# Kernel optimization log

Measured on AMD Instinct MI355X. Metric: run time of the kernel, lower is better.

Reference implementation:

```python
import jax, jax.numpy as jnp
import numpy as np

H = 32          # num_attention_heads
KVH = 8         # num_key_value_heads
D = 2048        # hidden_size
HD = D // H     # attention_head_size = 64
REP = H // KVH  # queries per kv head = 4


def setup_inputs() -> dict:
    key = jax.random.key(0)
    ks = jax.random.split(key, 7)
    s = 0.02
    return {
        "hidden_states": jax.random.normal(ks[0], (2, 2048, D), dtype=jnp.float32),
        "Wq": jax.random.normal(ks[1], (D, D), dtype=jnp.float32) * s,
        "bq": jax.random.normal(ks[2], (D,), dtype=jnp.float32) * s,
        "Wk": jax.random.normal(ks[3], (D, KVH * HD), dtype=jnp.float32) * s,
        "bk": jax.random.normal(ks[4], (KVH * HD,), dtype=jnp.float32) * s,
        "Wv": jax.random.normal(ks[5], (D, KVH * HD), dtype=jnp.float32) * s,
        "bv": jax.random.normal(ks[6], (KVH * HD,), dtype=jnp.float32) * s,
    }


def _split_heads(x, n_heads):
    # [B, S, n_heads*HD] -> [B, n_heads, S, HD]
    b, s, _ = x.shape
    return x.reshape(b, s, n_heads, HD).transpose(0, 2, 1, 3)


def reference(hidden_states, Wq, bq, Wk, bk, Wv, bv):
    b, s, _ = hidden_states.shape
    q = _split_heads(hidden_states @ Wq + bq, H)          # [B,H,S,HD]
    k = _split_heads(hidden_states @ Wk + bk, KVH)        # [B,KVH,S,HD]
    v = _split_heads(hidden_states @ Wv + bv, KVH)
    # repeat KV heads to match query heads (q_idx // REP -> kv_idx)
    k = jnp.repeat(k, REP, axis=1)                         # [B,H,S,HD]
    v = jnp.repeat(v, REP, axis=1)
    scores = jnp.einsum("bhqd,bhkd->bhqk", q, k) / jnp.sqrt(jnp.float32(HD))
    probs = jax.nn.softmax(scores, axis=-1)
    ctx = jnp.einsum("bhqk,bhkd->bhqd", probs, v)          # [B,H,S,HD]
    ctx = ctx.transpose(0, 2, 1, 3).reshape(b, s, H * HD)
    return ctx
```

## Files before the change

### kernel.cpp

```cpp
#include <hip/hip_runtime.h>
#include <hip/hip_bf16.h>

#define NH 32
#define NKVH 8
#define DMODEL 2048
#define HDIM 64
#define NB 2
#define SEQ 2048
#define MROWS (NB*SEQ)
#define NQ 2048
#define NKV 512
#define NTOT 3072
#define NT (SEQ/64)

typedef __bf16 bf16x4 __attribute__((ext_vector_type(4)));
typedef __bf16 bf16x8 __attribute__((ext_vector_type(8)));
typedef float  f32x2  __attribute__((ext_vector_type(2)));
typedef float  f32x4  __attribute__((ext_vector_type(4)));
typedef float  f32x16 __attribute__((ext_vector_type(16)));
typedef unsigned u32x2 __attribute__((ext_vector_type(2)));
typedef unsigned u32x4 __attribute__((ext_vector_type(4)));

__device__ inline __bf16 f2bf(float f) {
    unsigned u = __builtin_bit_cast(unsigned, f);
    u += 0x7fff + ((u >> 16) & 1);
    unsigned short s = (unsigned short)(u >> 16);
    return __builtin_bit_cast(__bf16, s);
}

__device__ inline unsigned pack2bf(float a, float b) {
    unsigned ua = __builtin_bit_cast(unsigned, a);
    ua += 0x7fff + ((ua >> 16) & 1);
    unsigned ub = __builtin_bit_cast(unsigned, b);
    ub += 0x7fff + ((ub >> 16) & 1);
    return (ua >> 16) | (ub & 0xffff0000u);
}

__device__ inline void gload_lds16(const void* g, void* l) {
    __builtin_amdgcn_global_load_lds(
        (const __attribute__((address_space(1))) void*)g,
        (__attribute__((address_space(3))) void*)l, 16, 0, 0);
}

__device__ inline float max3f(float a, float b, float c) {
    float r;
    asm("v_max3_f32 %0, %1, %2, %3" : "=v"(r) : "v"(a), "v"(b), "v"(c));
    return r;
}

__device__ inline float cross_max32(float x) {
#if __has_builtin(__builtin_amdgcn_permlane32_swap)
    unsigned xu = __builtin_bit_cast(unsigned, x);
    u32x2 r = __builtin_amdgcn_permlane32_swap(xu, xu, false, false);
    return fmaxf(__builtin_bit_cast(float, r[0]), __builtin_bit_cast(float, r[1]));
#else
    return fmaxf(x, __shfl_xor(x, 32));
#endif
}

__global__ __launch_bounds__(256)
void cvt_hs(const float* __restrict__ Hs, __bf16* __restrict__ Ab)
{
    size_t idx = ((size_t)blockIdx.x * 256 + threadIdx.x) * 8;
    f32x4 a = *reinterpret_cast<const f32x4*>(Hs + idx);
    f32x4 b = *reinterpret_cast<const f32x4*>(Hs + idx + 4);
    u32x4 w;
    w[0] = pack2bf(a[0], a[1]); w[1] = pack2bf(a[2], a[3]);
    w[2] = pack2bf(b[0], b[1]); w[3] = pack2bf(b[2], b[3]);
    *reinterpret_cast<u32x4*>((char*)Ab + idx * 2) = w;
}

__global__ __launch_bounds__(256)
void transpose_w(const float* __restrict__ Wq,
                 const float* __restrict__ Wk,
                 const float* __restrict__ Wv,
                 __bf16* __restrict__ Wt)
{
    __shared__ __bf16 tile[64][72];
    int k0 = blockIdx.x * 64;
    int n0 = blockIdx.y * 64;
    const float* Wsrc; int ncols; int nbase;
    if (n0 < NQ)            { Wsrc = Wq; ncols = NQ;  nbase = n0; }
    else if (n0 < NQ + NKV) { Wsrc = Wk; ncols = NKV; nbase = n0 - NQ; }
    else                    { Wsrc = Wv; ncols = NKV; nbase = n0 - NQ - NKV; }
    int t = threadIdx.x;
    int kl = t >> 2;
    int nc = (t & 3) * 16;
    const float* src = Wsrc + (size_t)(k0 + kl) * ncols + nbase + nc;
    #pragma unroll
    for (int i = 0; i < 4; ++i) {
        f32x4 v = *reinterpret_cast<const f32x4*>(src + i * 4);
        #pragma unroll
        for (int e = 0; e < 4; ++e) tile[kl][nc + i * 4 + e] = f2bf(v[e]);
    }
    __syncthreads();
    int nl = t >> 2;
    int kc = (t & 3) * 16;
    bf16x8 o0, o1;
    #pragma unroll
    for (int i = 0; i < 8; ++i) o0[i] = tile[kc + i][nl];
    #pragma unroll
    for (int i = 0; i < 8; ++i) o1[i] = tile[kc + 8 + i][nl];
    __bf16* dst = Wt + (size_t)(n0 + nl) * DMODEL + k0 + kc;
    *reinterpret_cast<bf16x8*>(dst)     = o0;
    *reinterpret_cast<bf16x8*>(dst + 8) = o1;
}

#define BM 128
#define BN 128
#define BK 64

__global__ __launch_bounds__(256)
void qkv_gemm(const __bf16* __restrict__ Ab,
              const __bf16* __restrict__ Wt,
              const float* __restrict__ bq,
              const float* __restrict__ bk,
              const float* __restrict__ bv,
              __bf16* __restrict__ Qb,
              __bf16* __restrict__ Kb,
              __bf16* __restrict__ Vt)
{
    __shared__ char lds[32768];

    int bid = blockIdx.x;
    int wg = (bid & 7) * 96 + (bid >> 3);
    int n0 = (wg % 24) * BN;
    int m0 = (wg / 24) * BM;

    int t = threadIdx.x;
    int wave = t >> 6, lane = t & 63;
    int g = lane >> 4, lh = lane & 15;
    int wr = wave >> 1, wc = wave & 1;

    int srow = wave * 8 + (lane >> 3);
    int schunk = (lane & 7) ^ (lane >> 3);
    const char* Asrc = (const char*)Ab + (size_t)(m0 + srow) * 4096 + schunk * 16;
    const char* Bsrc = (const char*)Wt + (size_t)(n0 + srow) * 4096 + schunk * 16;
    int dstw = wave * 1024;

    f32x4 acc[4][4] = {};

    for (int k0 = 0; k0 < DMODEL * 2; k0 += BK * 2) {
        #pragma unroll
        for (int i = 0; i < 4; ++i)
            gload_lds16(Asrc + (size_t)i * 32 * 4096 + k0, lds + i * 4096 + dstw);
        #pragma unroll
        for (int i = 0; i < 4; ++i)
            gload_lds16(Bsrc + (size_t)i * 32 * 4096 + k0, lds + 16384 + i * 4096 + dstw);
        __syncthreads();
        #pragma unroll
        for (int kk = 0; kk < 2; ++kk) {
            bf16x8 af[4], bfr[4];
            #pragma unroll
            for (int mi = 0; mi < 4; ++mi) {
                int row = wr * 64 + mi * 16 + lh;
                int byte = row * 128 + (((kk * 4 + g) ^ (lh & 7)) << 4);
                af[mi] = *reinterpret_cast<const bf16x8*>(lds + byte);
            }
            #pragma unroll
            for (int ni = 0; ni < 4; ++ni) {
                int row = wc * 64 + ni * 16 + lh;
                int byte = row * 128 + (((kk * 4 + g) ^ (lh & 7)) << 4);
                bfr[ni] = *reinterpret_cast<const bf16x8*>(lds + 16384 + byte);
            }
            #pragma unroll
            for (int mi = 0; mi < 4; ++mi)
                #pragma unroll
                for (int ni = 0; ni < 4; ++ni)
                    acc[mi][ni] = __builtin_amdgcn_mfma_f32_16x16x32_bf16(af[mi], bfr[ni], acc[mi][ni], 0, 0, 0);
        }
        __syncthreads();
    }

    int mode = (n0 < NQ) ? 0 : (n0 < NQ + NKV ? 1 : 2);
    const float* bias = (mode == 0) ? bq : (mode == 1 ? bk : bv);
    int nsub = (mode == 0) ? 0 : (mode == 1 ? NQ : NQ + NKV);
    float scale = (mode == 0) ? 0.18033688011112042f : 1.0f;

    float biasv[4];
    #pragma unroll
    for (int ni = 0; ni < 4; ++ni)
        biasv[ni] = bias[n0 - nsub + wc * 64 + ni * 16 + lh];

    #pragma unroll
    for (int mi = 0; mi < 4; ++mi) {
        #pragma unroll
        for (int j = 0; j < 4; ++j) {
            int m = m0 + wr * 64 + mi * 16 + 4 * g + j;
            int bb = m >> 11, s = m & (SEQ - 1);
            #pragma unroll
            for (int ni = 0; ni < 4; ++ni) {
                int n = n0 + wc * 64 + ni * 16 + lh;
                __bf16 val = f2bf((acc[mi][ni][j] + biasv[ni]) * scale);
                if (mode == 0) {
                    int hh = n >> 6, d = n & 63;
                    Qb[(((size_t)bb * NH + hh) * SEQ + s) * HDIM + d] = val;
                } else if (mode == 1) {
                    int nk = n - NQ; int kv = nk >> 6, d = nk & 63;
                    Kb[(((size_t)bb * NKVH + kv) * SEQ + s) * HDIM + d] = val;
                } else {
                    int nv = n - NQ - NKV; int kv = nv >> 6, d = nv & 63;
                    Vt[(((size_t)bb * NKVH + kv) * HDIM + d) * SEQ + s] = val;
                }
            }
        }
    }
}

#define SUBSTEP(BUFB, SS) do { \
    bf16x8 kf0_ = *reinterpret_cast<const bf16x8*>(lds + (BUFB) + koff[(SS)*4 + 0]); \
    bf16x8 kf1_ = *reinterpret_cast<const bf16x8*>(lds + (BUFB) + koff[(SS)*4 + 1]); \
    bf16x8 kf2_ = *reinterpret_cast<const bf16x8*>(lds + (BUFB) + koff[(SS)*4 + 2]); \
    bf16x8 kf3_ = *reinterpret_cast<const bf16x8*>(lds + (BUFB) + koff[(SS)*4 + 3]); \
    f32x16 s_ = {}; \
    __builtin_amdgcn_s_setprio(1); \
    s_ = __builtin_amdgcn_mfma_f32_32x32x16_bf16(kf0_, qf[0], s_, 0, 0, 0); \
    s_ = __builtin_amdgcn_mfma_f32_32x32x16_bf16(kf1_, qf[1], s_, 0, 0, 0); \
    s_ = __builtin_amdgcn_mfma_f32_32x32x16_bf16(kf2_, qf[2], s_, 0, 0, 0); \
    s_ = __builtin_amdgcn_mfma_f32_32x32x16_bf16(kf3_, qf[3], s_, 0, 0, 0); \
    __builtin_amdgcn_s_setprio(0); \
    float n0_ = max3f(max3f(s_[0], s_[1], s_[2]),  max3f(s_[3], s_[4], s_[5]), \
                      max3f(s_[6], s_[7], s_[8])); \
    float n1_ = max3f(max3f(s_[9], s_[10], s_[11]), max3f(s_[12], s_[13], s_[14]), s_[15]); \
    float mt_ = cross_max32(fmaxf(n0_, n1_)); \
    if (!__all(mt_ <= m_run + 8.0f)) { \
        float mn_ = fmaxf(m_run, mt_); \
        float al_ = __builtin_amdgcn_exp2f(m_run - mn_); \
        m_run = mn_; msub = -mn_; \
        accO0 *= al_; accO1 *= al_; lsum *= al_; \
    } \
    _Pragma("unroll") \
    for (int r = 0; r < 16; ++r) s_[r] = __builtin_amdgcn_exp2f(s_[r] + msub); \
    bf16x8 pa_, pb_; \
    _Pragma("unroll") \
    for (int e = 0; e < 8; ++e) { pa_[e] = (__bf16)s_[e]; pb_[e] = (__bf16)s_[8 + e]; } \
    bf16x8 va0_ = *reinterpret_cast<const bf16x8*>(lds + (BUFB) + 8192 + koff[2 * (SS)]); \
    bf16x8 vb0_ = *reinterpret_cast<const bf16x8*>(lds + (BUFB) + 8192 + koff[2 * (SS) + 1]); \
    bf16x8 va1_ = *reinterpret_cast<const bf16x8*>(lds + (BUFB) + 8192 + koff[4 + 2 * (SS)]); \
    bf16x8 vb1_ = *reinterpret_cast<const bf16x8*>(lds + (BUFB) + 8192 + koff[4 + 2 * (SS) + 1]); \
    __builtin_amdgcn_s_setprio(1); \
    accO0 = __builtin_amdgcn_mfma_f32_32x32x16_bf16(va0_, pa_, accO0, 0, 0, 0); \
    lsum  = __builtin_amdgcn_mfma_f32_32x32x16_bf16(ones, pa_, lsum,  0, 0, 0); \
    accO0 = __builtin_amdgcn_mfma_f32_32x32x16_bf16(vb0_, pb_, accO0, 0, 0, 0); \
    lsum  = __builtin_amdgcn_mfma_f32_32x32x16_bf16(ones, pb_, lsum,  0, 0, 0); \
    accO1 = __builtin_amdgcn_mfma_f32_32x32x16_bf16(va1_, pa_, accO1, 0, 0, 0); \
    accO1 = __builtin_amdgcn_mfma_f32_32x32x16_bf16(vb1_, pb_, accO1, 0, 0, 0); \
    __builtin_amdgcn_s_setprio(0); \
} while (0)

#define TILE(BUFB, NBUFB, KT, MORE) do { \
    if (MORE) { \
        const char* gk_ = Kp + (size_t)((KT) + 1) * 8192; \
        gload_lds16(gk_ + kgoff0, lds + (NBUFB) + kdst0); \
        gload_lds16(gk_ + kgoff1, lds + (NBUFB) + kdst1); \
        const char* gv_ = Vp + vgoff + (size_t)((KT) + 1) * 128; \
        v0r = *reinterpret_cast<const bf16x8*>(gv_); \
        v1r = *reinterpret_cast<const bf16x8*>(gv_ + 16); \
    } \
    SUBSTEP(BUFB, 0); \
    SUBSTEP(BUFB, 1); \
    if (MORE) { \
        bf16x8 cA_ = __builtin_shufflevector(v0r, v1r, 0, 1, 2, 3, 8, 9, 10, 11); \
        bf16x8 cB_ = __builtin_shufflevector(v0r, v1r, 4, 5, 6, 7, 12, 13, 14, 15); \
        *reinterpret_cast<bf16x8*>(lds + (NBUFB) + vwoffA)        = cA_; \
        *reinterpret_cast<bf16x8*>(lds + (NBUFB) + (vwoffA ^ 16)) = cB_; \
    } \
    __syncthreads(); \
} while (0)

__global__ __launch_bounds__(256, 3)
void attn(const __bf16* __restrict__ Qb,
          const __bf16* __restrict__ Kb,
          const __bf16* __restrict__ Vt,
          float* __restrict__ out)
{
    __shared__ char lds[32768];

    int qt = blockIdx.x;
    int bh = blockIdx.y;
    int b = bh >> 5, h = bh & 31;
    int kvh = h >> 2;
    int tid = threadIdx.x, wave = tid >> 6, lane = tid & 63;
    int ql = lane & 31, hi = lane >> 5;
    int q0 = qt * 128 + wave * 32;

    const __bf16* Qp = Qb + (size_t)(b * NH + h) * SEQ * HDIM;
    const char*   Kp = (const char*)(Kb + (size_t)(b * NKVH + kvh) * SEQ * HDIM);
    const char*   Vp = (const char*)(Vt + (size_t)(b * NKVH + kvh) * HDIM * SEQ);

    bf16x8 qf[4];
    #pragma unroll
    for (int f = 0; f < 4; ++f)
        qf[f] = *reinterpret_cast<const bf16x8*>(Qp + (size_t)(q0 + ql) * HDIM + f * 16 + hi * 8);

    u32x4 ou = { 0x3F803F80u, 0x3F803F80u, 0x3F803F80u, 0x3F803F80u };
    bf16x8 ones = __builtin_bit_cast(bf16x8, ou);

    int Mq = (ql & 7) << 4;
    int kgoff0 = wave * 1024 + ((lane >> 3) << 7) + (((lane & 7) ^ (lane >> 3)) << 4);
    int kgoff1 = kgoff0 + 4096;
    int kdst0 = wave * 1024;
    int kdst1 = kdst0 + 4096;
    int vd = wave * 16 + (lane >> 2);
    int vc = lane & 3;
    size_t vgoff = (size_t)vd * (SEQ * 2) + vc * 32;
    int Mv = (vd & 7) << 4;
    int vwoffA = 8192 + vd * 128 + ((vc * 32) ^ Mv);
    int koff[8];
    #pragma unroll
    for (int kb = 0; kb < 2; ++kb)
        #pragma unroll
        for (int f = 0; f < 4; ++f)
            koff[kb * 4 + f] = (kb * 32 + ql) * 128 + ((f * 32 + hi * 16) ^ Mq);

    f32x16 accO0 = {}, accO1 = {}, lsum = {};
    float m_run = -1e30f, msub = 0.0f;

    bf16x8 v0r, v1r;

    gload_lds16(Kp + kgoff0, lds + kdst0);
    gload_lds16(Kp + kgoff1, lds + kdst1);
    {
        const char* gv = Vp + vgoff;
        v0r = *reinterpret_cast<const bf16x8*>(gv);
        v1r = *reinterpret_cast<const bf16x8*>(gv + 16);
        bf16x8 cA = __builtin_shufflevector(v0r, v1r, 0, 1, 2, 3, 8, 9, 10, 11);
        bf16x8 cB = __builtin_shufflevector(v0r, v1r, 4, 5, 6, 7, 12, 13, 14, 15);
        *reinterpret_cast<bf16x8*>(lds + vwoffA)        = cA;
        *reinterpret_cast<bf16x8*>(lds + (vwoffA ^ 16)) = cB;
    }
    __syncthreads();

    #pragma unroll 1
    for (int kt2 = 0; kt2 < 15; ++kt2) {
        TILE(0,     16384, 2 * kt2,     true);
        TILE(16384, 0,     2 * kt2 + 1, true);
    }
    TILE(0,     16384, 30, true);
    TILE(16384, 0,     31, false);

    float inv = 1.0f / lsum[0];
    float* op = out + ((size_t)b * SEQ + q0 + ql) * DMODEL + h * HDIM;
    #pragma unroll
    for (int G = 0; G < 4; ++G) {
        f32x4 o0 = { accO0[4 * G + 0] * inv, accO0[4 * G + 1] * inv,
                     accO0[4 * G + 2] * inv, accO0[4 * G + 3] * inv };
        f32x4 o1 = { accO1[4 * G + 0] * inv, accO1[4 * G + 1] * inv,
                     accO1[4 * G + 2] * inv, accO1[4 * G + 3] * inv };
        *reinterpret_cast<f32x4*>(op + 8 * G + 4 * hi)      = o0;
        *reinterpret_cast<f32x4*>(op + 32 + 8 * G + 4 * hi) = o1;
    }
}

extern "C" void kernel_launch(void* const* d_in, const int* in_sizes, int n_in,
                              void* d_out, int out_size, void* d_ws, size_t ws_size,
                              hipStream_t stream)
{
    const float* hs = (const float*)d_in[0];
    const float* Wq = (const float*)d_in[1];
    const float* bq = (const float*)d_in[2];
    const float* Wk = (const float*)d_in[3];
    const float* bk = (const float*)d_in[4];
    const float* Wv = (const float*)d_in[5];
    const float* bv = (const float*)d_in[6];
    float* out = (float*)d_out;

    char* ws = (char*)d_ws;
    __bf16* Wt = (__bf16*)(ws);
    __bf16* Ab = (__bf16*)(ws + 12582912);
    __bf16* Qb = (__bf16*)(ws + 12582912 + 16777216);
    __bf16* Kb = (__bf16*)(ws + 12582912 + 2*16777216);
    __bf16* Vt = (__bf16*)(ws + 12582912 + 2*16777216 + 4194304);

    hipLaunchKernelGGL(cvt_hs,      dim3(4096),   dim3(256), 0, stream, hs, Ab);
    hipLaunchKernelGGL(transpose_w, dim3(32, 48), dim3(256), 0, stream, Wq, Wk, Wv, Wt);
    hipLaunchKernelGGL(qkv_gemm,    dim3(768),    dim3(256), 0, stream, Ab, Wt, bq, bk, bv, Qb, Kb, Vt);
    hipLaunchKernelGGL(attn,        dim3(16, 64), dim3(256), 0, stream, Qb, Kb, Vt, out);
}
```

Before: 189.5 us.

## Pre-permute V in GEMM epilogue, load V directly to LDS, use 512-thread blocks

The QKV GEMM epilogue now writes V^T with a permuted sequence order inside each 16-element group. This lets the attention kernel bring V tiles straight into LDS with the same global-to-LDS async copies used for K, so the register round trip, shuffles and LDS stores are gone. The attention block also grows to 8 waves (256 query rows) sharing each K/V tile. That halves the tile loads per query row, but the larger block raises register pressure at launch bounds (512,4) and adds barrier cost across more waves.

```diff
diff --git a/kernel.cpp b/kernel.cpp
--- a/kernel.cpp
+++ b/kernel.cpp
@@ -182,6 +182,8 @@
     for (int ni = 0; ni < 4; ++ni)
         biasv[ni] = bias[n0 - nsub + wc * 64 + ni * 16 + lh];
 
+    int gsw = ((g & 1) << 1) | (g >> 1);
+
     #pragma unroll
     for (int mi = 0; mi < 4; ++mi) {
         #pragma unroll
@@ -200,7 +202,8 @@
                     Kb[(((size_t)bb * NKVH + kv) * SEQ + s) * HDIM + d] = val;
                 } else {
                     int nv = n - NQ - NKV; int kv = nv >> 6, d = nv & 63;
-                    Vt[(((size_t)bb * NKVH + kv) * HDIM + d) * SEQ + s] = val;
+                    int sv = (s & ~12) | (gsw << 2);
+                    Vt[(((size_t)bb * NKVH + kv) * HDIM + d) * SEQ + sv] = val;
                 }
             }
         }
@@ -250,25 +253,15 @@
 
 #define TILE(BUFB, NBUFB, KT, MORE) do { \
     if (MORE) { \
-        const char* gk_ = Kp + (size_t)((KT) + 1) * 8192; \
-        gload_lds16(gk_ + kgoff0, lds + (NBUFB) + kdst0); \
-        gload_lds16(gk_ + kgoff1, lds + (NBUFB) + kdst1); \
-        const char* gv_ = Vp + vgoff + (size_t)((KT) + 1) * 128; \
-        v0r = *reinterpret_cast<const bf16x8*>(gv_); \
-        v1r = *reinterpret_cast<const bf16x8*>(gv_ + 16); \
+        gload_lds16(Kp + (size_t)((KT) + 1) * 8192 + kgoff, lds + (NBUFB) + kdst); \
+        gload_lds16(Vp + (size_t)((KT) + 1) * 128 + vgoff,  lds + (NBUFB) + vdst); \
     } \
     SUBSTEP(BUFB, 0); \
     SUBSTEP(BUFB, 1); \
-    if (MORE) { \
-        bf16x8 cA_ = __builtin_shufflevector(v0r, v1r, 0, 1, 2, 3, 8, 9, 10, 11); \
-        bf16x8 cB_ = __builtin_shufflevector(v0r, v1r, 4, 5, 6, 7, 12, 13, 14, 15); \
-        *reinterpret_cast<bf16x8*>(lds + (NBUFB) + vwoffA)        = cA_; \
-        *reinterpret_cast<bf16x8*>(lds + (NBUFB) + (vwoffA ^ 16)) = cB_; \
-    } \
     __syncthreads(); \
 } while (0)
 
-__global__ __launch_bounds__(256, 3)
+__global__ __launch_bounds__(512, 4)
 void attn(const __bf16* __restrict__ Qb,
           const __bf16* __restrict__ Kb,
           const __bf16* __restrict__ Vt,
@@ -282,7 +275,7 @@
     int kvh = h >> 2;
     int tid = threadIdx.x, wave = tid >> 6, lane = tid & 63;
     int ql = lane & 31, hi = lane >> 5;
-    int q0 = qt * 128 + wave * 32;
+    int q0 = qt * 256 + wave * 32;
 
     const __bf16* Qp = Qb + (size_t)(b * NH + h) * SEQ * HDIM;
     const char*   Kp = (const char*)(Kb + (size_t)(b * NKVH + kvh) * SEQ * HDIM);
@@ -296,39 +289,25 @@
     u32x4 ou = { 0x3F803F80u, 0x3F803F80u, 0x3F803F80u, 0x3F803F80u };
     bf16x8 ones = __builtin_bit_cast(bf16x8, ou);
 
-    int Mq = (ql & 7) << 4;
-    int kgoff0 = wave * 1024 + ((lane >> 3) << 7) + (((lane & 7) ^ (lane >> 3)) << 4);
-    int kgoff1 = kgoff0 + 4096;
-    int kdst0 = wave * 1024;
-    int kdst1 = kdst0 + 4096;
-    int vd = wave * 16 + (lane >> 2);
-    int vc = lane & 3;
-    size_t vgoff = (size_t)vd * (SEQ * 2) + vc * 32;
-    int Mv = (vd & 7) << 4;
-    int vwoffA = 8192 + vd * 128 + ((vc * 32) ^ Mv);
+    int srow = tid >> 3;
+    int schk = (tid & 7) ^ (srow & 7);
+    int kgoff = srow * 128 + (schk << 4);
+    size_t vgoff = (size_t)srow * (SEQ * 2) + (schk << 4);
+    int kdst = tid * 16;
+    int vdst = 8192 + tid * 16;
+
     int koff[8];
     #pragma unroll
     for (int kb = 0; kb < 2; ++kb)
         #pragma unroll
         for (int f = 0; f < 4; ++f)
-            koff[kb * 4 + f] = (kb * 32 + ql) * 128 + ((f * 32 + hi * 16) ^ Mq);
+            koff[kb * 4 + f] = (kb * 32 + ql) * 128 + ((f * 32 + hi * 16) ^ ((ql & 7) << 4));
 
     f32x16 accO0 = {}, accO1 = {}, lsum = {};
     float m_run = -1e30f, msub = 0.0f;
 
-    bf16x8 v0r, v1r;
-
-    gload_lds16(Kp + kgoff0, lds + kdst0);
-    gload_lds16(Kp + kgoff1, lds + kdst1);
-    {
-        const char* gv = Vp + vgoff;
-        v0r = *reinterpret_cast<const bf16x8*>(gv);
-        v1r = *reinterpret_cast<const bf16x8*>(gv + 16);
-        bf16x8 cA = __builtin_shufflevector(v0r, v1r, 0, 1, 2, 3, 8, 9, 10, 11);
-        bf16x8 cB = __builtin_shufflevector(v0r, v1r, 4, 5, 6, 7, 12, 13, 14, 15);
-        *reinterpret_cast<bf16x8*>(lds + vwoffA)        = cA;
-        *reinterpret_cast<bf16x8*>(lds + (vwoffA ^ 16)) = cB;
-    }
+    gload_lds16(Kp + kgoff, lds + kdst);
+    gload_lds16(Vp + vgoff, lds + vdst);
     __syncthreads();
 
     #pragma unroll 1
@@ -375,5 +354,5 @@
     hipLaunchKernelGGL(cvt_hs,      dim3(4096),   dim3(256), 0, stream, hs, Ab);
     hipLaunchKernelGGL(transpose_w, dim3(32, 48), dim3(256), 0, stream, Wq, Wk, Wv, Wt);
     hipLaunchKernelGGL(qkv_gemm,    dim3(768),    dim3(256), 0, stream, Ab, Wt, bq, bk, bv, Qb, Kb, Vt);
-    hipLaunchKernelGGL(attn,        dim3(16, 64), dim3(256), 0, stream, Qb, Kb, Vt, out);
-}
+    hipLaunchKernelGGL(attn,        dim3(8, 64),  dim3(512), 0, stream, Qb, Kb, Vt, out);
+}
```

After: 179.7 us. -5.2%, faster.
